# Optimization experiments

Hardware: AMD Instinct MI355X
Metric: run time of the kernel (lower is better)

The kernel has to match this reference:

```python
import jax, jax.numpy as jnp
import numpy as np

NTYPE, NWAVE, NIPS = 4, 8, 3
NUMATOM, NPAIR = 20000, 1000000
CUTOFF = 5.0
NUM_OC = 2
# index_para: angular-block id for each of the 1+3+9=13 angular channels
INDEX_PARA = jnp.array([0] + [1] * 3 + [2] * 9, dtype=jnp.int32)


def setup_inputs() -> dict:
    key = jax.random.key(0)
    ks = jax.random.split(key, 10)
    cart = jax.random.normal(ks[0], (NUMATOM, 3), dtype=jnp.float32) * 3.0
    neigh_list = jax.random.randint(ks[1], (2, NPAIR), 0, NUMATOM)
    shifts = jax.random.normal(ks[2], (NPAIR, 3), dtype=jnp.float32)
    species = jax.random.randint(ks[3], (NUMATOM,), 0, NTYPE)
    rs = jax.random.uniform(ks[4], (NTYPE, NWAVE), dtype=jnp.float32) * CUTOFF
    inta = jax.random.uniform(ks[5], (NTYPE, NWAVE), dtype=jnp.float32) + 0.5
    params = jax.random.normal(ks[6], (NTYPE, NWAVE * NIPS), dtype=jnp.float32)
    hyper = jax.random.normal(ks[7], (NUM_OC + 1, NIPS, NWAVE, NWAVE), dtype=jnp.float32)
    hyper = hyper / jnp.linalg.norm(hyper, axis=2, keepdims=True)  # F.normalize(dim=2)
    D = NWAVE * NIPS
    ocW = jax.random.normal(ks[8], (NUM_OC, D, D), dtype=jnp.float32) / np.sqrt(D)
    ocEmb = jax.random.normal(ks[9], (NUM_OC, NTYPE, D), dtype=jnp.float32)
    return {"cart": cart, "shifts": shifts, "rs": rs, "inta": inta,
            "params": params, "hyper": hyper, "ocW": ocW, "ocEmb": ocEmb,
            "neigh_list": neigh_list, "species": species}


def _forward(cart, shifts, rs, inta, params, hyper, ocW, ocEmb, neigh_list, species):
    numatom = cart.shape[0]
    i_center, j_neigh = neigh_list[0], neigh_list[1]
    neigh_species = species[j_neigh]                       # (P,)
    dvec = cart[i_center] - cart[j_neigh] - shifts         # (P,3)
    dist = jnp.linalg.norm(dvec, axis=-1)                  # (P,)
    u = dvec / dist[:, None]
    # cutoff_cosine
    cut = jnp.square(0.5 * jnp.cos(dist * (np.pi / CUTOFF)) + 0.5)
    # species-gathered Gaussian radial basis (vectorized per-type loop)
    radial = jnp.exp(-inta[neigh_species] * jnp.square(dist[:, None] - rs[neigh_species]))  # (P,nwave)
    # angular: [1, u, u (x) u] -> (P,13)
    ang = jnp.concatenate([jnp.ones((u.shape[0], 1), u.dtype), u,
                           (u[:, :, None] * u[:, None, :]).reshape(-1, 9)], axis=1)
    orbital = ang[:, :, None] * cut[:, None, None] * radial[:, None, :]  # (P,13,nwave)

    def obtain(hyp, orb_coeff):
        # hyp: (NIPS,nwave,nwave); orb_coeff: (numatom, NIPS*nwave)
        ep = orb_coeff.reshape(numatom, NIPS, NWAVE)[j_neigh][:, INDEX_PARA]  # (P,13,nwave)
        ep1 = hyp[INDEX_PARA]                                                 # (13,nwave,nwave)
        w = jnp.einsum('ijk,jkm->ijm', orbital, ep1) * ep                     # (P,13,nwave)
        sw = jax.ops.segment_sum(w, i_center, num_segments=numatom)           # (A,13,nwave)
        pd = jnp.square(sw)
        den = jax.ops.segment_sum(pd.transpose(1, 0, 2), INDEX_PARA,
                                  num_segments=NIPS).transpose(1, 0, 2)       # (A,NIPS,nwave)
        return den.reshape(numatom, -1)

    orb_coeff = params[species]                            # (A, NIPS*nwave)
    density = obtain(hyper[0], orb_coeff)
    for i in range(ocW.shape[0]):
        orb_coeff = jnp.tanh(density @ ocW[i] + ocEmb[i][species]) + orb_coeff
        density = obtain(hyper[i + 1], orb_coeff)
    return density


def reference(cart, shifts, rs, inta, params, hyper, ocW, ocEmb, neigh_list, species):
    return _forward(cart, shifts, rs, inta, params, hyper, ocW, ocEmb, neigh_list, species)
```

## Files before the change

### kernel.cpp

```cpp
#include <hip/hip_runtime.h>
#include <hip/hip_fp16.h>
#include <math.h>

#define NWAVE 8
#define OCD 24
#define CAP 96

struct __align__(16) Rec {
    __half u[4];
    __half cr[8];
    int jn;
    int pad;
};


__global__ __launch_bounds__(256) void fill_kernel(
    const int* __restrict__ nl, const float* __restrict__ cart,
    const float* __restrict__ shifts, const int* __restrict__ species,
    const float* __restrict__ rs, const float* __restrict__ inta,
    int* __restrict__ cnt, Rec* __restrict__ rec, int npair) {
    int p = blockIdx.x * blockDim.x + threadIdx.x;
    if (p >= npair) return;
    int i = nl[p];
    int j = nl[npair + p];
    int rank = atomicAdd(&cnt[i], 1);
    float dx = cart[3 * i + 0] - cart[3 * j + 0] - shifts[3 * p + 0];
    float dy = cart[3 * i + 1] - cart[3 * j + 1] - shifts[3 * p + 1];
    float dz = cart[3 * i + 2] - cart[3 * j + 2] - shifts[3 * p + 2];
    float dist = sqrtf(dx * dx + dy * dy + dz * dz);
    float inv = 1.0f / dist;
    float c = 0.5f * __cosf(dist * 0.62831853071795864769f) + 0.5f;
    float cut = c * c;
    int sj = species[j];
    Rec r;
    r.u[0] = __float2half(dx * inv);
    r.u[1] = __float2half(dy * inv);
    r.u[2] = __float2half(dz * inv);
    r.u[3] = __float2half(0.f);
#pragma unroll
    for (int k = 0; k < 8; ++k) {
        float dd = dist - rs[sj * 8 + k];
        r.cr[k] = __float2half(cut * __expf(-inta[sj * 8 + k] * dd * dd));
    }
    r.jn = j;
    r.pad = 0;
    if (rank < CAP) {
        int4* dst = (int4*)&rec[(size_t)i * CAP + rank];
        const int4* src = (const int4*)&r;
        dst[0] = src[0];
        dst[1] = src[1];
    }
}


__global__ void init_oc_kernel(const float* __restrict__ params, const int* __restrict__ species,
                               float* __restrict__ oc, int numatom) {
    int idx = blockIdx.x * blockDim.x + threadIdx.x;
    if (idx >= numatom * OCD) return;
    int a = idx / OCD, d = idx - a * OCD;
    oc[idx] = params[species[a] * OCD + d];
}

__global__ void update_kernel(const float* __restrict__ density,
                              const float* __restrict__ W,
                              const float* __restrict__ emb,
                              const int* __restrict__ species,
                              float* __restrict__ oc, int numatom) {
    int idx = blockIdx.x * blockDim.x + threadIdx.x;
    if (idx >= numatom * OCD) return;
    int a = idx / OCD, d = idx - a * OCD;
    const float* dens = density + a * OCD;
    float s = emb[species[a] * OCD + d];
#pragma unroll
    for (int e = 0; e < OCD; ++e) s += dens[e] * W[e * OCD + d];
    oc[idx] = tanhf(s) + oc[idx];
}


__global__ __launch_bounds__(256) void obtain_kernel(
    const Rec* __restrict__ rec, const int* __restrict__ cnt,
    const float* __restrict__ oc, const float* __restrict__ hyp,
    float* __restrict__ density,
    int numatom) {
    int wave = (int)((blockIdx.x * (size_t)blockDim.x + threadIdx.x) >> 6);
    if (wave >= numatom) return;
    int lane = threadIdx.x & 63;
    int m = lane & 7;
    int pp = lane >> 3;

    float hr[3][8];
#pragma unroll
    for (int ip = 0; ip < 3; ++ip)
#pragma unroll
        for (int k = 0; k < 8; ++k) hr[ip][k] = hyp[(ip * 8 + k) * 8 + m];

    float acc[13];
#pragma unroll
    for (int j = 0; j < 13; ++j) acc[j] = 0.f;

    int e = cnt[wave];
    e = e < CAP ? e : CAP;
    const Rec* base = rec + (size_t)wave * CAP;
    for (int p = pp; p < e; p += 8) {
        const int4* R = (const int4*)&base[p];
        int4 lo = R[0];
        int4 hi = R[1];
        const __half* hl = (const __half*)&lo;
        const __half* hh = (const __half*)&hi;
        float ux = __half2float(hl[0]);
        float uy = __half2float(hl[1]);
        float uz = __half2float(hl[2]);
        float cr[8];
#pragma unroll
        for (int k = 0; k < 4; ++k) cr[k] = __half2float(hl[4 + k]);
#pragma unroll
        for (int k = 0; k < 4; ++k) cr[4 + k] = __half2float(hh[k]);
        int jn = ((const int*)&hi)[2];
        float rh0 = 0.f, rh1 = 0.f, rh2 = 0.f;
#pragma unroll
        for (int k = 0; k < 8; ++k) {
            rh0 += cr[k] * hr[0][k];
            rh1 += cr[k] * hr[1][k];
            rh2 += cr[k] * hr[2][k];
        }
        const float* ocj = oc + jn * OCD;
        float t0 = rh0 * ocj[m];
        float t1 = rh1 * ocj[8 + m];
        float t2 = rh2 * ocj[16 + m];
        acc[0] += t0;
        acc[1] += ux * t1;
        acc[2] += uy * t1;
        acc[3] += uz * t1;
        float vx = ux * t2, vy = uy * t2, vz = uz * t2;
        acc[4] += ux * vx;
        acc[5] += ux * vy;
        acc[6] += ux * vz;
        acc[7] += uy * vx;
        acc[8] += uy * vy;
        acc[9] += uy * vz;
        acc[10] += uz * vx;
        acc[11] += uz * vy;
        acc[12] += uz * vz;
    }
#pragma unroll
    for (int j = 0; j < 13; ++j) {
        acc[j] += __shfl_xor(acc[j], 8);
        acc[j] += __shfl_xor(acc[j], 16);
        acc[j] += __shfl_xor(acc[j], 32);
    }
    if (pp == 0) {
        float d0 = acc[0] * acc[0];
        float d1 = acc[1] * acc[1] + acc[2] * acc[2] + acc[3] * acc[3];
        float d2 = 0.f;
#pragma unroll
        for (int j = 4; j < 13; ++j) d2 += acc[j] * acc[j];
        density[wave * OCD + m] = d0;
        density[wave * OCD + 8 + m] = d1;
        density[wave * OCD + 16 + m] = d2;
    }
}


extern "C" void kernel_launch(void* const* d_in, const int* in_sizes, int n_in,
                              void* d_out, int out_size, void* d_ws, size_t ws_size,
                              hipStream_t stream) {
    const float* cart = (const float*)d_in[0];
    const float* shifts = (const float*)d_in[1];
    const float* rs = (const float*)d_in[2];
    const float* inta = (const float*)d_in[3];
    const float* params = (const float*)d_in[4];
    const float* hyper = (const float*)d_in[5];
    const float* ocW = (const float*)d_in[6];
    const float* ocEmb = (const float*)d_in[7];
    const int* nl = (const int*)d_in[8];
    const int* species = (const int*)d_in[9];

    int numatom = in_sizes[0] / 3;
    int npair = in_sizes[8] / 2;
    int ntype = in_sizes[2] / NWAVE;

    char* w = (char*)d_ws;
    Rec* rec = (Rec*)w;
    size_t rec_bytes = (size_t)numatom * CAP * sizeof(Rec);
    int* cnt = (int*)(w + rec_bytes);
    float* oc = (float*)(cnt + numatom);
    float* density = (float*)d_out;

    const int tb = 256;
    hipMemsetAsync(cnt, 0, numatom * sizeof(int), stream);
    fill_kernel<<<(npair + tb - 1) / tb, tb, 0, stream>>>(nl, cart, shifts, species, rs, inta,
                                                          cnt, rec, npair);
    init_oc_kernel<<<(numatom * OCD + tb - 1) / tb, tb, 0, stream>>>(params, species, oc, numatom);

    int obl = (int)(((size_t)numatom * 64 + tb - 1) / tb);
    obtain_kernel<<<obl, tb, 0, stream>>>(rec, cnt, oc, hyper + 0 * 192, density, numatom);
    for (int it = 0; it < 2; ++it) {
        update_kernel<<<(numatom * OCD + tb - 1) / tb, tb, 0, stream>>>(
            density, ocW + (size_t)it * OCD * OCD, ocEmb + (size_t)it * ntype * OCD, species, oc,
            numatom);
        obtain_kernel<<<obl, tb, 0, stream>>>(rec, cnt, oc, hyper + (size_t)(it + 1) * 192,
                                              density, numatom);
    }
}
```

Before: 236.2 us.

## Split pair binning into scatter and slot-ordered build, prefetch records in obtain

The fused fill kernel is split in two. A scatter kernel atomically bins pair indices per center atom. A build kernel then iterates over atom slots, computes each record and writes it contiguously, so record stores become coalesced instead of scattered. The obtain loop is also software-pipelined: it loads the next record before processing the current one, to hide load latency. This adds a launch, a perm array and an extra indirect gather of shifts and neighbor indices. The build kernel also launches threads for all numatom*CAP slots, many of which return early.

```diff
diff --git a/kernel.cpp b/kernel.cpp
--- a/kernel.cpp
+++ b/kernel.cpp
@@ -14,42 +14,56 @@
 };
 
 
-__global__ __launch_bounds__(256) void fill_kernel(
+__global__ __launch_bounds__(256) void scatter_kernel(
+    const int* __restrict__ nl, int* __restrict__ cnt, int* __restrict__ perm, int npair) {
+    int p = blockIdx.x * 256 + threadIdx.x;
+    if (p >= npair) return;
+    int i = nl[p];
+    int rank = atomicAdd(&cnt[i], 1);
+    if (rank < CAP) perm[i * CAP + rank] = p;
+}
+
+
+__global__ __launch_bounds__(256) void build_kernel(
     const int* __restrict__ nl, const float* __restrict__ cart,
     const float* __restrict__ shifts, const int* __restrict__ species,
     const float* __restrict__ rs, const float* __restrict__ inta,
-    int* __restrict__ cnt, Rec* __restrict__ rec, int npair) {
-    int p = blockIdx.x * blockDim.x + threadIdx.x;
-    if (p >= npair) return;
-    int i = nl[p];
+    const int* __restrict__ cnt, const int* __restrict__ perm,
+    Rec* __restrict__ rec, int numatom, int npair) {
+    int s = blockIdx.x * 256 + threadIdx.x;
+    if (s >= numatom * CAP) return;
+    int a = s / CAP;
+    int r = s - a * CAP;
+    int e = cnt[a];
+    e = e < CAP ? e : CAP;
+    if (r >= e) return;
+    int p = perm[s];
     int j = nl[npair + p];
-    int rank = atomicAdd(&cnt[i], 1);
-    float dx = cart[3 * i + 0] - cart[3 * j + 0] - shifts[3 * p + 0];
-    float dy = cart[3 * i + 1] - cart[3 * j + 1] - shifts[3 * p + 1];
-    float dz = cart[3 * i + 2] - cart[3 * j + 2] - shifts[3 * p + 2];
+    float sx = shifts[3 * p + 0], sy = shifts[3 * p + 1], sz = shifts[3 * p + 2];
+    float dx = cart[3 * a + 0] - cart[3 * j + 0] - sx;
+    float dy = cart[3 * a + 1] - cart[3 * j + 1] - sy;
+    float dz = cart[3 * a + 2] - cart[3 * j + 2] - sz;
     float dist = sqrtf(dx * dx + dy * dy + dz * dz);
     float inv = 1.0f / dist;
     float c = 0.5f * __cosf(dist * 0.62831853071795864769f) + 0.5f;
     float cut = c * c;
     int sj = species[j];
-    Rec r;
-    r.u[0] = __float2half(dx * inv);
-    r.u[1] = __float2half(dy * inv);
-    r.u[2] = __float2half(dz * inv);
-    r.u[3] = __float2half(0.f);
+    Rec rc;
+    rc.u[0] = __float2half(dx * inv);
+    rc.u[1] = __float2half(dy * inv);
+    rc.u[2] = __float2half(dz * inv);
+    rc.u[3] = __float2half(0.f);
 #pragma unroll
     for (int k = 0; k < 8; ++k) {
         float dd = dist - rs[sj * 8 + k];
-        r.cr[k] = __float2half(cut * __expf(-inta[sj * 8 + k] * dd * dd));
-    }
-    r.jn = j;
-    r.pad = 0;
-    if (rank < CAP) {
-        int4* dst = (int4*)&rec[(size_t)i * CAP + rank];
-        const int4* src = (const int4*)&r;
-        dst[0] = src[0];
-        dst[1] = src[1];
-    }
+        rc.cr[k] = __float2half(cut * __expf(-inta[sj * 8 + k] * dd * dd));
+    }
+    rc.jn = j;
+    rc.pad = 0;
+    int4* dst = (int4*)&rec[s];
+    const int4* src = (const int4*)&rc;
+    dst[0] = src[0];
+    dst[1] = src[1];
 }
 
 
@@ -100,47 +114,64 @@
 
     int e = cnt[wave];
     e = e < CAP ? e : CAP;
-    const Rec* base = rec + (size_t)wave * CAP;
-    for (int p = pp; p < e; p += 8) {
-        const int4* R = (const int4*)&base[p];
-        int4 lo = R[0];
-        int4 hi = R[1];
-        const __half* hl = (const __half*)&lo;
-        const __half* hh = (const __half*)&hi;
-        float ux = __half2float(hl[0]);
-        float uy = __half2float(hl[1]);
-        float uz = __half2float(hl[2]);
-        float cr[8];
-#pragma unroll
-        for (int k = 0; k < 4; ++k) cr[k] = __half2float(hl[4 + k]);
-#pragma unroll
-        for (int k = 0; k < 4; ++k) cr[4 + k] = __half2float(hh[k]);
-        int jn = ((const int*)&hi)[2];
-        float rh0 = 0.f, rh1 = 0.f, rh2 = 0.f;
-#pragma unroll
-        for (int k = 0; k < 8; ++k) {
-            rh0 += cr[k] * hr[0][k];
-            rh1 += cr[k] * hr[1][k];
-            rh2 += cr[k] * hr[2][k];
+    const int4* base = (const int4*)(rec + (size_t)wave * CAP);
+
+    int p = pp;
+    if (p < e) {
+        int4 lo = base[2 * p];
+        int4 hi = base[2 * p + 1];
+        while (true) {
+            int pn = p + 8;
+            bool more = pn < e;
+            int4 nlo, nhi;
+            if (more) {
+                nlo = base[2 * pn];
+                nhi = base[2 * pn + 1];
+            }
+            int jn = ((const int*)&hi)[2];
+            const float* ocj = oc + jn * OCD;
+            float o0 = ocj[m];
+            float o1 = ocj[8 + m];
+            float o2 = ocj[16 + m];
+            const __half* hl = (const __half*)&lo;
+            const __half* hh = (const __half*)&hi;
+            float ux = __half2float(hl[0]);
+            float uy = __half2float(hl[1]);
+            float uz = __half2float(hl[2]);
+            float cr[8];
+#pragma unroll
+            for (int k = 0; k < 4; ++k) cr[k] = __half2float(hl[4 + k]);
+#pragma unroll
+            for (int k = 0; k < 4; ++k) cr[4 + k] = __half2float(hh[k]);
+            float rh0 = 0.f, rh1 = 0.f, rh2 = 0.f;
+#pragma unroll
+            for (int k = 0; k < 8; ++k) {
+                rh0 += cr[k] * hr[0][k];
+                rh1 += cr[k] * hr[1][k];
+                rh2 += cr[k] * hr[2][k];
+            }
+            float t0 = rh0 * o0;
+            float t1 = rh1 * o1;
+            float t2 = rh2 * o2;
+            acc[0] += t0;
+            acc[1] += ux * t1;
+            acc[2] += uy * t1;
+            acc[3] += uz * t1;
+            float vx = ux * t2, vy = uy * t2, vz = uz * t2;
+            acc[4] += ux * vx;
+            acc[5] += ux * vy;
+            acc[6] += ux * vz;
+            acc[7] += uy * vx;
+            acc[8] += uy * vy;
+            acc[9] += uy * vz;
+            acc[10] += uz * vx;
+            acc[11] += uz * vy;
+            acc[12] += uz * vz;
+            if (!more) break;
+            p = pn;
+            lo = nlo;
+            hi = nhi;
         }
-        const float* ocj = oc + jn * OCD;
-        float t0 = rh0 * ocj[m];
-        float t1 = rh1 * ocj[8 + m];
-        float t2 = rh2 * ocj[16 + m];
-        acc[0] += t0;
-        acc[1] += ux * t1;
-        acc[2] += uy * t1;
-        acc[3] += uz * t1;
-        float vx = ux * t2, vy = uy * t2, vz = uz * t2;
-        acc[4] += ux * vx;
-        acc[5] += ux * vy;
-        acc[6] += ux * vz;
-        acc[7] += uy * vx;
-        acc[8] += uy * vy;
-        acc[9] += uy * vz;
-        acc[10] += uz * vx;
-        acc[11] += uz * vy;
-        acc[12] += uz * vz;
     }
 #pragma unroll
     for (int j = 0; j < 13; ++j) {
@@ -182,14 +213,16 @@
     char* w = (char*)d_ws;
     Rec* rec = (Rec*)w;
     size_t rec_bytes = (size_t)numatom * CAP * sizeof(Rec);
-    int* cnt = (int*)(w + rec_bytes);
+    int* perm = (int*)(w + rec_bytes);
+    int* cnt = perm + (size_t)numatom * CAP;
     float* oc = (float*)(cnt + numatom);
     float* density = (float*)d_out;
 
     const int tb = 256;
     hipMemsetAsync(cnt, 0, numatom * sizeof(int), stream);
-    fill_kernel<<<(npair + tb - 1) / tb, tb, 0, stream>>>(nl, cart, shifts, species, rs, inta,
-                                                          cnt, rec, npair);
+    scatter_kernel<<<(npair + tb - 1) / tb, tb, 0, stream>>>(nl, cnt, perm, npair);
+    build_kernel<<<(numatom * CAP + tb - 1) / tb, tb, 0, stream>>>(
+        nl, cart, shifts, species, rs, inta, cnt, perm, rec, numatom, npair);
     init_oc_kernel<<<(numatom * OCD + tb - 1) / tb, tb, 0, stream>>>(params, species, oc, numatom);
 
     int obl = (int)(((size_t)numatom * 64 + tb - 1) / tb);
```

Result: slower. 274.4 us (+16.2%).

## Interleave orbital coefficients as float4 per wave and prefetch next pair in obtain

Applied to the files above, without the earlier changes.

Orbital coefficients are stored per atom as 8 float4 slots (one per radial wave m) holding the three angular-block values, so each obtain lane gathers one 16-byte vector instead of three scattered floats. The obtain loop is software-pipelined so the next record and its neighbour's coefficients are loaded before the current pair is processed, hiding gather latency. The update and init kernels write the new layout. This uses about a third more workspace for the padded layout and holds more registers for the prefetch.

```diff
diff --git a/kernel.cpp b/kernel.cpp
--- a/kernel.cpp
+++ b/kernel.cpp
@@ -19,7 +19,7 @@
     const float* __restrict__ shifts, const int* __restrict__ species,
     const float* __restrict__ rs, const float* __restrict__ inta,
     int* __restrict__ cnt, Rec* __restrict__ rec, int npair) {
-    int p = blockIdx.x * blockDim.x + threadIdx.x;
+    int p = blockIdx.x * 256 + threadIdx.x;
     if (p >= npair) return;
     int i = nl[p];
     int j = nl[npair + p];
@@ -53,19 +53,20 @@
 }
 
 
-__global__ void init_oc_kernel(const float* __restrict__ params, const int* __restrict__ species,
-                               float* __restrict__ oc, int numatom) {
+__global__ void init_ocp_kernel(const float* __restrict__ params, const int* __restrict__ species,
+                                float4* __restrict__ ocp, int numatom) {
     int idx = blockIdx.x * blockDim.x + threadIdx.x;
-    if (idx >= numatom * OCD) return;
-    int a = idx / OCD, d = idx - a * OCD;
-    oc[idx] = params[species[a] * OCD + d];
+    if (idx >= numatom * 8) return;
+    int a = idx >> 3, m = idx & 7;
+    const float* pr = params + species[a] * OCD;
+    ocp[idx] = make_float4(pr[m], pr[8 + m], pr[16 + m], 0.f);
 }
 
 __global__ void update_kernel(const float* __restrict__ density,
                               const float* __restrict__ W,
                               const float* __restrict__ emb,
                               const int* __restrict__ species,
-                              float* __restrict__ oc, int numatom) {
+                              float* __restrict__ ocp, int numatom) {
     int idx = blockIdx.x * blockDim.x + threadIdx.x;
     if (idx >= numatom * OCD) return;
     int a = idx / OCD, d = idx - a * OCD;
@@ -73,13 +74,14 @@
     float s = emb[species[a] * OCD + d];
 #pragma unroll
     for (int e = 0; e < OCD; ++e) s += dens[e] * W[e * OCD + d];
-    oc[idx] = tanhf(s) + oc[idx];
+    int slot = a * 32 + (d & 7) * 4 + (d >> 3);
+    ocp[slot] = tanhf(s) + ocp[slot];
 }
 
 
 __global__ __launch_bounds__(256) void obtain_kernel(
     const Rec* __restrict__ rec, const int* __restrict__ cnt,
-    const float* __restrict__ oc, const float* __restrict__ hyp,
+    const float4* __restrict__ ocp, const float* __restrict__ hyp,
     float* __restrict__ density,
     int numatom) {
     int wave = (int)((blockIdx.x * (size_t)blockDim.x + threadIdx.x) >> 6);
@@ -100,47 +102,63 @@
 
     int e = cnt[wave];
     e = e < CAP ? e : CAP;
-    const Rec* base = rec + (size_t)wave * CAP;
-    for (int p = pp; p < e; p += 8) {
-        const int4* R = (const int4*)&base[p];
-        int4 lo = R[0];
-        int4 hi = R[1];
-        const __half* hl = (const __half*)&lo;
-        const __half* hh = (const __half*)&hi;
-        float ux = __half2float(hl[0]);
-        float uy = __half2float(hl[1]);
-        float uz = __half2float(hl[2]);
-        float cr[8];
-#pragma unroll
-        for (int k = 0; k < 4; ++k) cr[k] = __half2float(hl[4 + k]);
-#pragma unroll
-        for (int k = 0; k < 4; ++k) cr[4 + k] = __half2float(hh[k]);
-        int jn = ((const int*)&hi)[2];
-        float rh0 = 0.f, rh1 = 0.f, rh2 = 0.f;
-#pragma unroll
-        for (int k = 0; k < 8; ++k) {
-            rh0 += cr[k] * hr[0][k];
-            rh1 += cr[k] * hr[1][k];
-            rh2 += cr[k] * hr[2][k];
+    const int4* base = (const int4*)(rec + (size_t)wave * CAP);
+
+    int p = pp;
+    if (p < e) {
+        int4 lo = base[2 * p];
+        int4 hi = base[2 * p + 1];
+        float4 oc_cur = ocp[(size_t)((const int*)&hi)[2] * 8 + m];
+        while (true) {
+            int pn = p + 8;
+            bool more = pn < e;
+            int4 nlo, nhi;
+            float4 oc_nxt;
+            if (more) {
+                nlo = base[2 * pn];
+                nhi = base[2 * pn + 1];
+                oc_nxt = ocp[(size_t)((const int*)&nhi)[2] * 8 + m];
+            }
+            const __half* hl = (const __half*)&lo;
+            const __half* hh = (const __half*)&hi;
+            float ux = __half2float(hl[0]);
+            float uy = __half2float(hl[1]);
+            float uz = __half2float(hl[2]);
+            float cr[8];
+#pragma unroll
+            for (int k = 0; k < 4; ++k) cr[k] = __half2float(hl[4 + k]);
+#pragma unroll
+            for (int k = 0; k < 4; ++k) cr[4 + k] = __half2float(hh[k]);
+            float rh0 = 0.f, rh1 = 0.f, rh2 = 0.f;
+#pragma unroll
+            for (int k = 0; k < 8; ++k) {
+                rh0 += cr[k] * hr[0][k];
+                rh1 += cr[k] * hr[1][k];
+                rh2 += cr[k] * hr[2][k];
+            }
+            float t0 = rh0 * oc_cur.x;
+            float t1 = rh1 * oc_cur.y;
+            float t2 = rh2 * oc_cur.z;
+            acc[0] += t0;
+            acc[1] += ux * t1;
+            acc[2] += uy * t1;
+            acc[3] += uz * t1;
+            float vx = ux * t2, vy = uy * t2, vz = uz * t2;
+            acc[4] += ux * vx;
+            acc[5] += ux * vy;
+            acc[6] += ux * vz;
+            acc[7] += uy * vx;
+            acc[8] += uy * vy;
+            acc[9] += uy * vz;
+            acc[10] += uz * vx;
+            acc[11] += uz * vy;
+            acc[12] += uz * vz;
+            if (!more) break;
+            p = pn;
+            lo = nlo;
+            hi = nhi;
+            oc_cur = oc_nxt;
         }
-        const float* ocj = oc + jn * OCD;
-        float t0 = rh0 * ocj[m];
-        float t1 = rh1 * ocj[8 + m];
-        float t2 = rh2 * ocj[16 + m];
-        acc[0] += t0;
-        acc[1] += ux * t1;
-        acc[2] += uy * t1;
-        acc[3] += uz * t1;
-        float vx = ux * t2, vy = uy * t2, vz = uz * t2;
-        acc[4] += ux * vx;
-        acc[5] += ux * vy;
-        acc[6] += ux * vz;
-        acc[7] += uy * vx;
-        acc[8] += uy * vy;
-        acc[9] += uy * vz;
-        acc[10] += uz * vx;
-        acc[11] += uz * vy;
-        acc[12] += uz * vz;
     }
 #pragma unroll
     for (int j = 0; j < 13; ++j) {
@@ -183,22 +201,22 @@
     Rec* rec = (Rec*)w;
     size_t rec_bytes = (size_t)numatom * CAP * sizeof(Rec);
     int* cnt = (int*)(w + rec_bytes);
-    float* oc = (float*)(cnt + numatom);
+    float4* ocp = (float4*)(cnt + ((numatom + 3) & ~3));
     float* density = (float*)d_out;
 
     const int tb = 256;
     hipMemsetAsync(cnt, 0, numatom * sizeof(int), stream);
     fill_kernel<<<(npair + tb - 1) / tb, tb, 0, stream>>>(nl, cart, shifts, species, rs, inta,
                                                           cnt, rec, npair);
-    init_oc_kernel<<<(numatom * OCD + tb - 1) / tb, tb, 0, stream>>>(params, species, oc, numatom);
+    init_ocp_kernel<<<(numatom * 8 + tb - 1) / tb, tb, 0, stream>>>(params, species, ocp, numatom);
 
     int obl = (int)(((size_t)numatom * 64 + tb - 1) / tb);
-    obtain_kernel<<<obl, tb, 0, stream>>>(rec, cnt, oc, hyper + 0 * 192, density, numatom);
+    obtain_kernel<<<obl, tb, 0, stream>>>(rec, cnt, ocp, hyper + 0 * 192, density, numatom);
     for (int it = 0; it < 2; ++it) {
         update_kernel<<<(numatom * OCD + tb - 1) / tb, tb, 0, stream>>>(
-            density, ocW + (size_t)it * OCD * OCD, ocEmb + (size_t)it * ntype * OCD, species, oc,
-            numatom);
-        obtain_kernel<<<obl, tb, 0, stream>>>(rec, cnt, oc, hyper + (size_t)(it + 1) * 192,
+            density, ocW + (size_t)it * OCD * OCD, ocEmb + (size_t)it * ntype * OCD, species,
+            (float*)ocp, numatom);
+        obtain_kernel<<<obl, tb, 0, stream>>>(rec, cnt, ocp, hyper + (size_t)(it + 1) * 192,
                                               density, numatom);
     }
 }
```

After: 255.4 us. +8.1%, slower.
